# Optimization experiments

Hardware: AMD Instinct MI355X
Metric: run time of the kernel (lower is better)

## Reference

```python
import jax, jax.numpy as jnp
import numpy as np
from jax import lax

RATIO = 4
NUM_UPS = 2  # log2(RATIO)

def _taps():
    cdf23 = 2.0 * np.array([0.5, 0.305334091185, 0.0, -0.072698593239, 0.0,
                            0.021809577942, 0.0, -0.005192756653, 0.0,
                            0.000807762146, 0.0, -6.0081482e-05])
    base = np.concatenate([cdf23[1:][::-1], cdf23])  # 23 symmetric taps
    return jnp.asarray(base, dtype=jnp.float32)

def _dwconv(x, kern, c):
    # depthwise cross-correlation, matches torch F.conv2d(groups=c)
    return lax.conv_general_dilated(
        x, kern, window_strides=(1, 1), padding='VALID',
        dimension_numbers=('NCHW', 'OIHW', 'NCHW'), feature_group_count=c)

def setup_inputs() -> dict:
    key = jax.random.key(0)
    x = jax.random.normal(key, (16, 8, 160, 160), dtype=jnp.float32)
    return {"x": x}

def reference(x) -> jnp.ndarray:
    taps = _taps()                      # [23]
    pad = (taps.shape[0] - 1) // 2      # 11
    bs, c, h, w = x.shape
    kw = jnp.tile(taps.reshape(1, 1, 1, -1), (c, 1, 1, 1))  # [c,1,1,23]
    kh = jnp.tile(taps.reshape(1, 1, -1, 1), (c, 1, 1, 1))  # [c,1,23,1]
    cur = x
    for k in range(NUM_UPS):
        h, w = h * 2, w * 2
        off = 1 if k == 0 else 0
        up = jnp.zeros((bs, c, h, w), dtype=x.dtype)
        up = up.at[..., off::2, off::2].set(cur)  # zero-insertion upsample
        # width pass: replicate pad + 1x23 depthwise conv
        pw = jnp.pad(up, ((0, 0), (0, 0), (0, 0), (pad, pad)), mode='edge')
        fw = _dwconv(pw, kw, c)
        # height pass: circular pad + 23x1 depthwise conv
        ph = jnp.pad(fw, ((0, 0), (0, 0), (pad, pad), (0, 0)), mode='wrap')
        cur = _dwconv(ph, kh, c)
    return cur
```

## Files before the change

### kernel.cpp

```cpp
#include <hip/hip_runtime.h>

typedef float v4f __attribute__((ext_vector_type(4)));

__device__ constexpr float W12[12] = {
    -1.20162964e-04f,    1.615524292e-03f, -1.0385513306e-02f,  4.3619155884e-02f,
    -1.45397186478e-01f, 6.1066818237e-01f, 6.1066818237e-01f, -1.45397186478e-01f,
     4.3619155884e-02f, -1.0385513306e-02f, 1.615524292e-03f,  -1.20162964e-04f
};

__device__ __forceinline__ int xcd_map(int bid, int nblk) {
    int cpx = nblk >> 3;
    return (bid & 7) * cpx + (bid >> 3);
}

__global__ __launch_bounds__(256) void k_fused(const float* __restrict__ x,
                                               float* __restrict__ out) {
    __shared__ float xw[32][84];
    __shared__ float meb[21][84];
    __shared__ float ew[43][132];

    int bid = xcd_map(blockIdx.x, gridDim.x);
    int ct = bid % 5, rt = (bid / 5) % 10, bc = bid / 50;
    int K0  = rt * 32;
    int MC0 = ct * 64;
    int XB  = K0 / 2 - 8;
    int tid = threadIdx.x;

#pragma unroll
    for (int it = 0; it < 2; ++it) {
        int idx = it * 256 + tid;
        int e = idx / 10, g = idx % 10;
        if (e < 32) {
            int m = XB + e;
            m = m < 0 ? m + 160 : (m >= 160 ? m - 160 : m);
            const float* xr = x + (bc * 160 + m) * 160;
            int qg = 8 * ct - 1 + g;
            int i0 = 4 * qg;
            float flat[20];
#pragma unroll
            for (int b = 0; b < 5; ++b) {
                int bq = qg - 2 + b; bq = bq < 0 ? 0 : (bq > 39 ? 39 : bq);
                *(v4f*)(flat + 4 * b) = *(const v4f*)(xr + 4 * bq);
            }
            if (ct == 0) {
#pragma unroll
                for (int p = 2; p < 8; ++p) flat[p] = (i0 - 8 + p < 0) ? 0.f : flat[p];
            }
            float xlast = flat[19];
            if (ct == 4) {
#pragma unroll
                for (int p = 12; p < 17; ++p) flat[p] = (i0 - 8 + p > 159) ? xlast : flat[p];
            }
            float f[4], cpy[4];
#pragma unroll
            for (int d = 0; d < 4; ++d) {
                float acc = 0.f;
#pragma unroll
                for (int s = 0; s < 12; ++s) acc += W12[s] * flat[d + s + 2];
                f[d] = acc;
                cpy[d] = flat[d + 8];
            }
            if (ct == 4 && i0 >= 151) {
#pragma unroll
                for (int d = 0; d < 4; ++d) {
                    int i = i0 + d;
                    float c = 0.f;
#pragma unroll
                    for (int s = 0; s < 12; ++s) if (i + s >= 165) c += W12[s];
                    cpy[d] += c * xlast;
                }
            }
            v4f o0, o1;
            o0.x = f[0]; o0.y = cpy[0]; o0.z = f[1]; o0.w = cpy[1];
            o1.x = f[2]; o1.y = cpy[2]; o1.z = f[3]; o1.w = cpy[3];
            *(v4f*)(&xw[e][8 * g])     = o0;
            *(v4f*)(&xw[e][8 * g + 4]) = o1;
        }
    }
    __syncthreads();

    {
        int p = tid / 20, lq = tid % 20;
        if (p < 11) {
            int rlast = 2 * p + 12; rlast = rlast < 32 ? rlast : 31;
            v4f r[13];
#pragma unroll
            for (int s = 0; s < 12; ++s) r[s] = *(const v4f*)(&xw[2 * p + s][4 * lq]);
            r[12] = *(const v4f*)(&xw[rlast][4 * lq]);
            v4f a0 = {0.f, 0.f, 0.f, 0.f}, a1 = {0.f, 0.f, 0.f, 0.f};
#pragma unroll
            for (int s = 0; s < 12; ++s) {
                a0 += W12[s] * r[s];
                a1 += W12[s] * r[s + 1];
            }
            *(v4f*)(&meb[2 * p][4 * lq]) = a0;
            if (2 * p + 1 < 21) *(v4f*)(&meb[2 * p + 1][4 * lq]) = a1;
        }
    }
    __syncthreads();

#pragma unroll
    for (int it = 0; it < 2; ++it) {
        int idx = it * 256 + tid;
        int e = idx >> 3, h = idx & 7;
        if (e < 43) {
            const float* row = (e & 1) ? &meb[(e - 1) / 2][0] : &xw[e / 2 + 5][0];
            float flat[24];
#pragma unroll
            for (int b = 0; b < 6; ++b)
                *(v4f*)(flat + 4 * b) = *(const v4f*)(row + 4 * (2 * h + b));
            float f[8], cpy[8];
            if (ct == 0 && h == 0) {
                float m0 = row[8];
#pragma unroll
                for (int p = 3; p < 8; ++p) flat[p] = m0;
#pragma unroll
                for (int d = 0; d < 8; ++d) {
                    float acc = 0.f;
#pragma unroll
                    for (int s = 0; s < 12; ++s) acc += W12[s] * flat[d + s + 3];
                    f[d] = acc;
                    cpy[d] = flat[d + 8];
                }
#pragma unroll
                for (int d = 0; d < 6; ++d) {
                    float c = 0.f;
#pragma unroll
                    for (int s = 0; s < 12; ++s) if (d + s <= 5) c += W12[s];
                    cpy[d] += c * m0;
                }
            } else {
                if (ct == 4 && h == 7) {
#pragma unroll
                    for (int p = 16; p < 24; ++p) flat[p] = 0.f;
                }
#pragma unroll
                for (int d = 0; d < 8; ++d) {
                    float acc = 0.f;
#pragma unroll
                    for (int s = 0; s < 12; ++s) acc += W12[s] * flat[d + s + 3];
                    f[d] = acc;
                    cpy[d] = flat[d + 8];
                }
            }
#pragma unroll
            for (int j = 0; j < 4; ++j) {
                v4f v;
                v.x = cpy[2 * j]; v.y = f[2 * j];
                v.z = cpy[2 * j + 1]; v.w = f[2 * j + 1];
                *(v4f*)(&ew[e][16 * h + 4 * j]) = v;
            }
        }
    }
    __syncthreads();

    {
        int c4 = tid & 31, slot = tid >> 5;
        int C0 = MC0 * 2;
        float* base = out + (size_t)bc * 640 * 640 + C0 + 4 * c4;
        v4f w[12];
#pragma unroll
        for (int t = 0; t < 12; ++t) w[t] = *(const v4f*)(&ew[slot * 4 + t][4 * c4]);
#pragma unroll
        for (int u = 0; u < 4; ++u) {
            if (u > 0) {
#pragma unroll
                for (int t = 0; t < 11; ++t) w[t] = w[t + 1];
                w[11] = *(const v4f*)(&ew[slot * 4 + u + 11][4 * c4]);
            }
            int kk = slot * 4 + u;
            __builtin_nontemporal_store(w[5],
                (v4f*)(base + (size_t)(2 * (K0 + kk)) * 640));
            v4f acc = W12[0] * w[0];
#pragma unroll
            for (int s = 1; s < 12; ++s) acc += W12[s] * w[s];
            __builtin_nontemporal_store(acc,
                (v4f*)(base + (size_t)(2 * (K0 + kk) + 1) * 640));
        }
    }
}

extern "C" void kernel_launch(void* const* d_in, const int* in_sizes, int n_in,
                              void* d_out, int out_size, void* d_ws, size_t ws_size,
                              hipStream_t stream) {
    const float* x = (const float*)d_in[0];
    float* out = (float*)d_out;
    k_fused<<<6400, 256, 0, stream>>>(x, out);
}
```

Before: 46.37 us.

## Split ew generation into two halves interleaved with output emission

The third stage (building the ew rows) is split into two chunks. The first chunk of rows is generated, then output rows 0-15 are emitted while the remaining ew rows are computed in the same phase, and finally rows 16-31 are emitted. The aim is to overlap global stores with LDS compute and to shorten the serialized phases, at the cost of less ILP per emit phase and more live registers per thread.

```diff
diff --git a/kernel.cpp b/kernel.cpp
--- a/kernel.cpp
+++ b/kernel.cpp
@@ -99,84 +99,96 @@
     }
     __syncthreads();
 
-#pragma unroll
-    for (int it = 0; it < 2; ++it) {
-        int idx = it * 256 + tid;
-        int e = idx >> 3, h = idx & 7;
-        if (e < 43) {
-            const float* row = (e & 1) ? &meb[(e - 1) / 2][0] : &xw[e / 2 + 5][0];
-            float flat[24];
-#pragma unroll
-            for (int b = 0; b < 6; ++b)
-                *(v4f*)(flat + 4 * b) = *(const v4f*)(row + 4 * (2 * h + b));
-            float f[8], cpy[8];
-            if (ct == 0 && h == 0) {
-                float m0 = row[8];
-#pragma unroll
-                for (int p = 3; p < 8; ++p) flat[p] = m0;
-#pragma unroll
-                for (int d = 0; d < 8; ++d) {
-                    float acc = 0.f;
-#pragma unroll
-                    for (int s = 0; s < 12; ++s) acc += W12[s] * flat[d + s + 3];
-                    f[d] = acc;
-                    cpy[d] = flat[d + 8];
-                }
-#pragma unroll
-                for (int d = 0; d < 6; ++d) {
-                    float c = 0.f;
-#pragma unroll
-                    for (int s = 0; s < 12; ++s) if (d + s <= 5) c += W12[s];
-                    cpy[d] += c * m0;
-                }
-            } else {
-                if (ct == 4 && h == 7) {
-#pragma unroll
-                    for (int p = 16; p < 24; ++p) flat[p] = 0.f;
-                }
-#pragma unroll
-                for (int d = 0; d < 8; ++d) {
-                    float acc = 0.f;
-#pragma unroll
-                    for (int s = 0; s < 12; ++s) acc += W12[s] * flat[d + s + 3];
-                    f[d] = acc;
-                    cpy[d] = flat[d + 8];
-                }
-            }
-#pragma unroll
-            for (int j = 0; j < 4; ++j) {
-                v4f v;
-                v.x = cpy[2 * j]; v.y = f[2 * j];
-                v.z = cpy[2 * j + 1]; v.w = f[2 * j + 1];
-                *(v4f*)(&ew[e][16 * h + 4 * j]) = v;
-            }
-        }
-    }
-    __syncthreads();
-
-    {
-        int c4 = tid & 31, slot = tid >> 5;
-        int C0 = MC0 * 2;
-        float* base = out + (size_t)bc * 640 * 640 + C0 + 4 * c4;
+    auto gen_ew = [&](int e, int h) {
+        const float* row = (e & 1) ? &meb[(e - 1) / 2][0] : &xw[e / 2 + 5][0];
+        float flat[24];
+#pragma unroll
+        for (int b = 0; b < 6; ++b)
+            *(v4f*)(flat + 4 * b) = *(const v4f*)(row + 4 * (2 * h + b));
+        float f[8], cpy[8];
+        if (ct == 0 && h == 0) {
+            float m0 = row[8];
+#pragma unroll
+            for (int p = 3; p < 8; ++p) flat[p] = m0;
+#pragma unroll
+            for (int d = 0; d < 8; ++d) {
+                float acc = 0.f;
+#pragma unroll
+                for (int s = 0; s < 12; ++s) acc += W12[s] * flat[d + s + 3];
+                f[d] = acc;
+                cpy[d] = flat[d + 8];
+            }
+#pragma unroll
+            for (int d = 0; d < 6; ++d) {
+                float c = 0.f;
+#pragma unroll
+                for (int s = 0; s < 12; ++s) if (d + s <= 5) c += W12[s];
+                cpy[d] += c * m0;
+            }
+        } else {
+            if (ct == 4 && h == 7) {
+#pragma unroll
+                for (int p = 16; p < 24; ++p) flat[p] = 0.f;
+            }
+#pragma unroll
+            for (int d = 0; d < 8; ++d) {
+                float acc = 0.f;
+#pragma unroll
+                for (int s = 0; s < 12; ++s) acc += W12[s] * flat[d + s + 3];
+                f[d] = acc;
+                cpy[d] = flat[d + 8];
+            }
+        }
+#pragma unroll
+        for (int j = 0; j < 4; ++j) {
+            v4f v;
+            v.x = cpy[2 * j]; v.y = f[2 * j];
+            v.z = cpy[2 * j + 1]; v.w = f[2 * j + 1];
+            *(v4f*)(&ew[e][16 * h + 4 * j]) = v;
+        }
+    };
+
+    int c4 = tid & 31, slot = tid >> 5;
+    float* dbase = out + (size_t)bc * 640 * 640 + 2 * MC0 + 4 * c4;
+    auto emit_pair = [&](const v4f* w, int kk) {
+        __builtin_nontemporal_store(w[5],
+            (v4f*)(dbase + (size_t)(2 * (K0 + kk)) * 640));
+        v4f acc = W12[0] * w[0];
+#pragma unroll
+        for (int s = 1; s < 12; ++s) acc += W12[s] * w[s];
+        __builtin_nontemporal_store(acc,
+            (v4f*)(dbase + (size_t)(2 * (K0 + kk) + 1) * 640));
+    };
+
+    {
+        int e = tid >> 3, h = tid & 7;
+        if (e < 27) gen_ew(e, h);
+    }
+    __syncthreads();
+
+    {
         v4f w[12];
 #pragma unroll
-        for (int t = 0; t < 12; ++t) w[t] = *(const v4f*)(&ew[slot * 4 + t][4 * c4]);
-#pragma unroll
-        for (int u = 0; u < 4; ++u) {
-            if (u > 0) {
-#pragma unroll
-                for (int t = 0; t < 11; ++t) w[t] = w[t + 1];
-                w[11] = *(const v4f*)(&ew[slot * 4 + u + 11][4 * c4]);
-            }
-            int kk = slot * 4 + u;
-            __builtin_nontemporal_store(w[5],
-                (v4f*)(base + (size_t)(2 * (K0 + kk)) * 640));
-            v4f acc = W12[0] * w[0];
-#pragma unroll
-            for (int s = 1; s < 12; ++s) acc += W12[s] * w[s];
-            __builtin_nontemporal_store(acc,
-                (v4f*)(base + (size_t)(2 * (K0 + kk) + 1) * 640));
-        }
+        for (int t = 0; t < 12; ++t) w[t] = *(const v4f*)(&ew[2 * slot + t][4 * c4]);
+        emit_pair(w, 2 * slot);
+#pragma unroll
+        for (int t = 0; t < 11; ++t) w[t] = w[t + 1];
+        w[11] = *(const v4f*)(&ew[2 * slot + 12][4 * c4]);
+        emit_pair(w, 2 * slot + 1);
+        int e = 27 + (tid >> 3), h = tid & 7;
+        if (e < 43) gen_ew(e, h);
+    }
+    __syncthreads();
+
+    {
+        v4f w[12];
+#pragma unroll
+        for (int t = 0; t < 12; ++t) w[t] = *(const v4f*)(&ew[16 + 2 * slot + t][4 * c4]);
+        emit_pair(w, 16 + 2 * slot);
+#pragma unroll
+        for (int t = 0; t < 11; ++t) w[t] = w[t + 1];
+        w[11] = *(const v4f*)(&ew[16 + 2 * slot + 12][4 * c4]);
+        emit_pair(w, 16 + 2 * slot + 1);
     }
 }
 
```

New measurement: 46.87 us. Within noise of the previous version (+1.1%).
